# Kernel tuning notes

Measured on AMD Instinct MI355X. Metric: run time of the kernel, lower is better.

The kernel has to match this reference:

```python
import jax, jax.numpy as jnp
import numpy as np

ALPHA = 0.2  # LeakyReLU negative slope


def setup_inputs() -> dict:
    key = jax.random.key(0)
    k1, k2, k3, k4 = jax.random.split(key, 4)
    B, N, Fin, Fout = 8, 2048, 256, 256
    h = jax.random.normal(k1, (B, N, Fin), dtype=jnp.float32)
    # random 0/1 adjacency with guaranteed self-loops so every row has a neighbor
    adj = jax.random.randint(k2, (N, N), 0, 2).astype(jnp.float32)
    adj = jnp.maximum(adj, jnp.eye(N, dtype=jnp.float32))
    # xavier_uniform with gain=1.414
    def xavier(k, shape, gain=1.414):
        fan_in, fan_out = shape[0], shape[1]
        a = gain * np.sqrt(6.0 / (fan_in + fan_out))
        return jax.random.uniform(k, shape, dtype=jnp.float32, minval=-a, maxval=a)
    W = xavier(k3, (Fin, Fout))
    a = xavier(k4, (2 * Fout, 1))
    return {"h": h, "adj_matrix": adj, "W": W, "a": a}


def reference(h, adj_matrix, W, a):
    # h: [B, N, Fin], adj_matrix: [N, N], W: [Fin, Fout], a: [2*Fout, 1]
    Fout = W.shape[1]
    Wh = jnp.einsum("bnf,fo->bno", h, W)            # [B, N, Fout]
    a1, a2 = a[:Fout, 0], a[Fout:, 0]                 # split additive attention vector
    # e[b,i,j] = leakyrelu(Wh[b,i]@a1 + Wh[b,j]@a2) — equals concat([Wh_i,Wh_j])@a
    s1 = Wh @ a1                                      # [B, N]
    s2 = Wh @ a2                                      # [B, N]
    e = s1[:, :, None] + s2[:, None, :]               # [B, N, N]
    e = jnp.where(e >= 0, e, ALPHA * e)               # LeakyReLU
    e = jnp.where(adj_matrix[None] == 0, -jnp.inf, e)  # mask non-edges
    attention = jax.nn.softmax(e, axis=-1)            # [B, N, N]
    # dropout is identity in eval mode (training=False)
    h_prime = jnp.einsum("bij,bjo->bio", attention, Wh)
    return h_prime
```

## Files before the change

kernel.cpp:

```cpp
#include <hip/hip_runtime.h>
#include <cstdint>

#define NN 2048
#define LOG2E 1.4426950408889634f

typedef __attribute__((ext_vector_type(8))) short bf16x8;
typedef __attribute__((ext_vector_type(4))) float f32x4;

__device__ __forceinline__ unsigned short f2bf(float x){
  union { float f; unsigned u; } v; v.f = x;
  unsigned r = v.u + 0x7FFFu + ((v.u >> 16) & 1u);
  return (unsigned short)(r >> 16);
}
__device__ __forceinline__ unsigned pack2(float a, float b){
  return (unsigned)f2bf(a) | ((unsigned)f2bf(b) << 16);
}
__device__ __forceinline__ unsigned permpack(unsigned hi, unsigned lo){
  return __builtin_amdgcn_perm(hi, lo, 0x07060302u);
}

__global__ __launch_bounds__(256) void k_prep(const float* __restrict__ adj,
                                              const float* __restrict__ W,
                                              unsigned long long* __restrict__ ab,
                                              unsigned short* __restrict__ Wt){
  const int tid = threadIdx.x;
  const int bid = blockIdx.x;
  if (bid < 512){
    const int lane = tid & 63;
    unsigned* ab32 = (unsigned*)ab;
    #pragma unroll
    for (int r = 0; r < 4; r++){
      const int row = bid * 4 + r;
      #pragma unroll
      for (int part = 0; part < 2; part++){
        float4 v = ((const float4*)(adj + (size_t)row * NN))[part * 256 + tid];
        unsigned n = (v.x != 0.f ? 1u : 0u) | (v.y != 0.f ? 2u : 0u)
                   | (v.z != 0.f ? 4u : 0u) | (v.w != 0.f ? 8u : 0u);
        unsigned m;
        m = __shfl_xor(n, 1); n = (lane & 1) ? (m | (n << 4))  : (n | (m << 4));
        m = __shfl_xor(n, 2); n = (lane & 2) ? (m | (n << 8))  : (n | (m << 8));
        m = __shfl_xor(n, 4); n = (lane & 4) ? (m | (n << 16)) : (n | (m << 16));
        if ((lane & 7) == 0)
          ab32[row * 64 + part * 32 + (tid >> 3)] = n;
      }
    }
  } else {
    int g = (bid - 512) * 256 + tid;
    int o = g >> 8, k = g & 255;
    Wt[g] = f2bf(W[k * 256 + o]);
  }
}

__global__ __launch_bounds__(512, 2) void k_fused_gemm(const float* __restrict__ h,
                                                       const unsigned short* __restrict__ Wt,
                                                       const float* __restrict__ a,
                                                       unsigned short* __restrict__ WhT,
                                                       float* __restrict__ s1c,
                                                       float* __restrict__ s2c){
  __shared__ __align__(16) unsigned char As[2 * 8192];
  __shared__ __align__(16) unsigned short Ts[256 * 72];
  __shared__ float s1p[8][64], s2p[8][64];
  const int tid = threadIdx.x;
  const int r0 = blockIdx.x * 64;
  const int b  = r0 >> 11;
  const int i0 = r0 & (NN - 1);
  const int w = tid >> 6, lane = tid & 63, lhi = lane >> 4, llo = lane & 15;
  const int wc = w * 32;
  const int sit = w >> 1, skk = w & 1;
  const int srow = sit * 16 + llo;
  const int skol = skk * 32 + lhi * 8;

  f32x4 acc[4][2];
  #pragma unroll
  for (int i = 0; i < 4; i++)
    #pragma unroll
    for (int j = 0; j < 2; j++){ acc[i][j][0]=0.f; acc[i][j][1]=0.f; acc[i][j][2]=0.f; acc[i][j][3]=0.f; }

  float4 hv[4][2];
  #pragma unroll
  for (int t = 0; t < 4; t++){
    const float* hp = h + (size_t)(r0 + srow) * 256 + t * 64 + skol;
    hv[t][0] = *(const float4*)hp;
    hv[t][1] = *(const float4*)(hp + 4);
  }

  auto loadB = [&](int k0, bf16x8* dst){
    #pragma unroll
    for (int ot = 0; ot < 2; ot++)
      #pragma unroll
      for (int kk = 0; kk < 2; kk++)
        dst[ot * 2 + kk] = *(const bf16x8*)(Wt + (size_t)(wc + ot * 16 + llo) * 256 + k0 + kk * 32 + lhi * 8);
  };
  bf16x8 bfr[2][4];
  loadB(0, bfr[0]);

  #pragma unroll
  for (int t = 0; t < 4; t++){
    uint4 q = make_uint4(pack2(hv[t][0].x, hv[t][0].y), pack2(hv[t][0].z, hv[t][0].w),
                         pack2(hv[t][1].x, hv[t][1].y), pack2(hv[t][1].z, hv[t][1].w));
    *(uint4*)&As[(t & 1) * 8192 + w * 1024 + lane * 16] = q;
    __syncthreads();
    if (t < 3) loadB((t + 1) * 64, bfr[(t + 1) & 1]);
    bf16x8 af[2][4];
    #pragma unroll
    for (int kk = 0; kk < 2; kk++)
      #pragma unroll
      for (int it = 0; it < 4; it++)
        af[kk][it] = *(const bf16x8*)&As[(t & 1) * 8192 + (it * 2 + kk) * 1024 + lane * 16];
    #pragma unroll
    for (int kk = 0; kk < 2; kk++)
      #pragma unroll
      for (int it = 0; it < 4; it++)
        #pragma unroll
        for (int ot = 0; ot < 2; ot++)
          acc[it][ot] = __builtin_amdgcn_mfma_f32_16x16x32_bf16(af[kk][it], bfr[t & 1][ot * 2 + kk], acc[it][ot], 0, 0, 0);
  }

  float a1v[2], a2v[2];
  #pragma unroll
  for (int ot = 0; ot < 2; ot++){
    a1v[ot] = a[wc + ot * 16 + llo] * LOG2E;
    a2v[ot] = a[256 + wc + ot * 16 + llo] * LOG2E;
  }
  #pragma unroll
  for (int it = 0; it < 4; it++){
    #pragma unroll
    for (int q = 0; q < 4; q++){
      float p1 = acc[it][0][q] * a1v[0] + acc[it][1][q] * a1v[1];
      float p2 = acc[it][0][q] * a2v[0] + acc[it][1][q] * a2v[1];
      #pragma unroll
      for (int o = 1; o < 16; o <<= 1){ p1 += __shfl_xor(p1, o); p2 += __shfl_xor(p2, o); }
      if (llo == 0){
        s1p[w][it * 16 + lhi * 4 + q] = p1;
        s2p[w][it * 16 + lhi * 4 + q] = p2;
      }
    }
  }

  #pragma unroll
  for (int it = 0; it < 4; it++){
    #pragma unroll
    for (int ot = 0; ot < 2; ot++){
      int o = wc + ot * 16 + llo;
      uint2 u = make_uint2(pack2(acc[it][ot][0], acc[it][ot][1]),
                           pack2(acc[it][ot][2], acc[it][ot][3]));
      *(uint2*)&Ts[o * 72 + it * 16 + lhi * 4] = u;
    }
  }
  __syncthreads();

  if (tid < 64){
    float t1 = 0.f, t2 = 0.f;
    #pragma unroll
    for (int g = 0; g < 8; g++){ t1 += s1p[g][tid]; t2 += s2p[g][tid]; }
    s1c[r0 + tid] = t1;
    s2c[r0 + tid] = t2;
  }
  #pragma unroll
  for (int p = 0; p < 4; p++){
    int o = p * 64 + (tid >> 3), col = (tid & 7) * 8;
    *(uint4*)(WhT + (size_t)(b * 256 + o) * 2048 + i0 + col) = *(const uint4*)&Ts[o * 72 + col];
  }
}

__global__ __launch_bounds__(512, 2) void k_attn(const float* __restrict__ s1c,
                                                 const float* __restrict__ s2c,
                                                 const unsigned short* __restrict__ WhT,
                                                 const unsigned long long* __restrict__ ab,
                                                 float* __restrict__ out){
  __shared__ __align__(16) float E1s[2048];
  __shared__ __align__(16) float E2s[2048];
  __shared__ __align__(16) unsigned char Ps[65536];
  __shared__ __align__(16) unsigned char bitsB[64 * 264];
  __shared__ float s1s[64], lin[64], red[8], rsp[8][64];
  const int tid = threadIdx.x;
  const int bid = blockIdx.x;
  const int b = bid & 7, i0 = (bid >> 3) * 64;
  const int w = tid >> 6, lane = tid & 63, lhi = lane >> 4, llo = lane & 15;
  const int wc = w * 32;
  const int sit = w >> 1, skk = w & 1;
  const int sfrag = sit * 2 + skk;
  const int prow = sit * 16 + llo;

  auto loadB = [&](int j0, bf16x8* dst){
    #pragma unroll
    for (int ot = 0; ot < 2; ot++)
      #pragma unroll
      for (int kk = 0; kk < 2; kk++)
        dst[ot * 2 + kk] = *(const bf16x8*)(WhT + (size_t)(b * 256 + wc + ot * 16 + llo) * 2048 + j0 + kk * 32 + lhi * 8);
  };
  bf16x8 bA[4], bB[4];
  loadB(0, bA);

  float4 v = ((const float4*)(s2c + (size_t)b * NN))[tid];
  ((float4*)E1s)[tid] = make_float4(__builtin_amdgcn_exp2f(v.x), __builtin_amdgcn_exp2f(v.y),
                                    __builtin_amdgcn_exp2f(v.z), __builtin_amdgcn_exp2f(v.w));
  ((float4*)E2s)[tid] = make_float4(__builtin_amdgcn_exp2f(0.2f * v.x), __builtin_amdgcn_exp2f(0.2f * v.y),
                                    __builtin_amdgcn_exp2f(0.2f * v.z), __builtin_amdgcn_exp2f(0.2f * v.w));
  float vmax = fmaxf(fmaxf(v.x, v.y), fmaxf(v.z, v.w));
  #pragma unroll
  for (int o = 32; o; o >>= 1) vmax = fmaxf(vmax, __shfl_xor(vmax, o));
  if (lane == 0) red[w] = vmax;
  if (tid < 64) s1s[tid] = s1c[(size_t)b * NN + i0 + tid];
  #pragma unroll
  for (int k = 0; k < 4; k++){
    int g = k * 512 + tid;
    unsigned long long mw = ab[(size_t)i0 * 32 + g];
    *(unsigned long long*)&bitsB[(g >> 5) * 264 + (g & 31) * 8] = mw;
  }
  __syncthreads();
  float m2 = red[0];
  #pragma unroll
  for (int g = 1; g < 8; g++) m2 = fmaxf(m2, red[g]);

  const float s1v = s1s[prow];
  const float xm = s1v + m2;
  const float mv = fmaxf(xm, 0.2f * xm);
  const float k1 = __builtin_amdgcn_exp2f(s1v - mv);
  const float k2 = __builtin_amdgcn_exp2f(0.2f * s1v - mv);
  float rs = 0.f;

  f32x4 acc[4][2];
  #pragma unroll
  for (int i = 0; i < 4; i++)
    #pragma unroll
    for (int j = 0; j < 2; j++){ acc[i][j][0]=0.f; acc[i][j][1]=0.f; acc[i][j][2]=0.f; acc[i][j][3]=0.f; }

  unsigned puq[32];
  auto computeP = [&](int sN, int jc, unsigned* pq){
    const int j0 = sN * 512 + jc * 64 + skk * 32 + lhi * 8;
    unsigned bits = bitsB[prow * 264 + (j0 >> 3)];
    float4 xa = *(const float4*)&E1s[j0];
    float4 xb = *(const float4*)&E1s[j0 + 4];
    float4 ya = *(const float4*)&E2s[j0];
    float4 yb = *(const float4*)&E2s[j0 + 4];
    float e1[8] = {xa.x, xa.y, xa.z, xa.w, xb.x, xb.y, xb.z, xb.w};
    float e2[8] = {ya.x, ya.y, ya.z, ya.w, yb.x, yb.y, yb.z, yb.w};
    unsigned pu[8];
    #pragma unroll
    for (int e = 0; e < 8; e++){
      float p = fmaxf(e1[e] * k1, e2[e] * k2);
      unsigned m = ((bits >> e) & 1u) ? 0xFFFF0000u : 0u;
      unsigned u = __float_as_uint(p) & m;
      rs += __uint_as_float(u);
      pu[e] = u;
    }
    pq[0] = permpack(pu[1], pu[0]); pq[1] = permpack(pu[3], pu[2]);
    pq[2] = permpack(pu[5], pu[4]); pq[3] = permpack(pu[7], pu[6]);
  };

  #pragma unroll
  for (int jc = 0; jc < 8; jc++) computeP(0, jc, &puq[jc * 4]);

  for (int s = 0; s < 4; s++){
    if (s) __syncthreads();
    #pragma unroll
    for (int jc = 0; jc < 8; jc++)
      *(uint4*)&Ps[jc * 8192 + sfrag * 1024 + lane * 16] = *(const uint4*)&puq[jc * 4];
    __syncthreads();
    #pragma unroll
    for (int jc = 0; jc < 8; jc++){
      bf16x8 af[2][4];
      #pragma unroll
      for (int kk = 0; kk < 2; kk++)
        #pragma unroll
        for (int it = 0; it < 4; it++)
          af[kk][it] = *(const bf16x8*)&Ps[jc * 8192 + (it * 2 + kk) * 1024 + lane * 16];
      bf16x8* cur = (jc & 1) ? bB : bA;
      bf16x8* nxt = (jc & 1) ? bA : bB;
      if (jc < 7)       loadB((s * 8 + jc + 1) * 64, nxt);
      else if (s < 3)   loadB((s + 1) * 512, nxt);
      if (s < 3) computeP(s + 1, jc, &puq[jc * 4]);
      __builtin_amdgcn_s_setprio(1);
      #pragma unroll
      for (int kk = 0; kk < 2; kk++)
        #pragma unroll
        for (int it = 0; it < 4; it++)
          #pragma unroll
          for (int ot = 0; ot < 2; ot++)
            acc[it][ot] = __builtin_amdgcn_mfma_f32_16x16x32_bf16(af[kk][it], cur[ot * 2 + kk], acc[it][ot], 0, 0, 0);
      __builtin_amdgcn_s_setprio(0);
    }
  }

  rs += __shfl_xor(rs, 16);
  rs += __shfl_xor(rs, 32);
  if (lhi == 0) rsp[w][prow] = rs;
  __syncthreads();
  if (tid < 64){
    int it = tid >> 4;
    lin[tid] = 1.0f / (rsp[it * 2][tid] + rsp[it * 2 + 1][tid]);
  }
  __syncthreads();

  #pragma unroll
  for (int it = 0; it < 4; it++){
    #pragma unroll
    for (int ot = 0; ot < 2; ot++){
      int col = wc + ot * 16 + llo;
      #pragma unroll
      for (int q = 0; q < 4; q++){
        int row = it * 16 + lhi * 4 + q;
        out[(size_t)(b * NN + i0 + row) * 256 + col] = acc[it][ot][q] * lin[row];
      }
    }
  }
}

extern "C" void kernel_launch(void* const* d_in, const int* in_sizes, int n_in,
                              void* d_out, int out_size, void* d_ws, size_t ws_size,
                              hipStream_t stream) {
  const float* h   = (const float*)d_in[0];
  const float* adj = (const float*)d_in[1];
  const float* W   = (const float*)d_in[2];
  const float* a   = (const float*)d_in[3];
  float* out = (float*)d_out;

  char* ws = (char*)d_ws;
  unsigned short* WhT      = (unsigned short*)(ws);
  unsigned short* Wt       = (unsigned short*)(ws + 8388608);
  unsigned long long* ab   = (unsigned long long*)(ws + 8519680);
  float* s1c               = (float*)(ws + 9043968);
  float* s2c               = (float*)(ws + 9109504);

  hipLaunchKernelGGL(k_prep,       dim3(768), dim3(256), 0, stream, adj, W, ab, Wt);
  hipLaunchKernelGGL(k_fused_gemm, dim3(256), dim3(512), 0, stream, h, Wt, a, WhT, s1c, s2c);
  hipLaunchKernelGGL(k_attn,       dim3(256), dim3(512), 0, stream, s1c, s2c, WhT, ab, out);
}
```

Baseline: 130.9 us.

## Compute attention probabilities per wave in registers, drop LDS P exchange

Each wave now computes the bf16 attention-probability fragments for all 64 rows itself, straight from the E1/E2 tables and the adjacency bits, and feeds them directly into MFMA. This removes the 64KB shared-memory P buffer and its block-wide barriers. Row sums now come from an extra MFMA against a ones vector instead of a shuffle and LDS reduction. The trade is that the exp/mask/pack work is repeated in all 8 waves (8x more VALU work) plus 50% more MFMAs, in exchange for lower LDS use, which may allow higher occupancy, and no synchronisation.

```diff
diff --git a/kernel.cpp b/kernel.cpp
--- a/kernel.cpp
+++ b/kernel.cpp
@@ -170,17 +170,13 @@
                                                  float* __restrict__ out){
   __shared__ __align__(16) float E1s[2048];
   __shared__ __align__(16) float E2s[2048];
-  __shared__ __align__(16) unsigned char Ps[65536];
   __shared__ __align__(16) unsigned char bitsB[64 * 264];
-  __shared__ float s1s[64], lin[64], red[8], rsp[8][64];
+  __shared__ float s1s[64], red[8];
   const int tid = threadIdx.x;
   const int bid = blockIdx.x;
   const int b = bid & 7, i0 = (bid >> 3) * 64;
   const int w = tid >> 6, lane = tid & 63, lhi = lane >> 4, llo = lane & 15;
   const int wc = w * 32;
-  const int sit = w >> 1, skk = w & 1;
-  const int sfrag = sit * 2 + skk;
-  const int prow = sit * 16 + llo;
 
   auto loadB = [&](int j0, bf16x8* dst){
     #pragma unroll
@@ -213,95 +209,80 @@
   #pragma unroll
   for (int g = 1; g < 8; g++) m2 = fmaxf(m2, red[g]);
 
-  const float s1v = s1s[prow];
-  const float xm = s1v + m2;
-  const float mv = fmaxf(xm, 0.2f * xm);
-  const float k1 = __builtin_amdgcn_exp2f(s1v - mv);
-  const float k2 = __builtin_amdgcn_exp2f(0.2f * s1v - mv);
-  float rs = 0.f;
-
-  f32x4 acc[4][2];
-  #pragma unroll
-  for (int i = 0; i < 4; i++)
+  float k1v[4], k2v[4];
+  #pragma unroll
+  for (int it = 0; it < 4; it++){
+    float s1v = s1s[it * 16 + llo];
+    float xm = s1v + m2;
+    float mv = fmaxf(xm, 0.2f * xm);
+    k1v[it] = __builtin_amdgcn_exp2f(s1v - mv);
+    k2v[it] = __builtin_amdgcn_exp2f(0.2f * s1v - mv);
+  }
+
+  f32x4 acc[4][2], accr[4];
+  #pragma unroll
+  for (int i = 0; i < 4; i++){
+    accr[i][0]=0.f; accr[i][1]=0.f; accr[i][2]=0.f; accr[i][3]=0.f;
     #pragma unroll
     for (int j = 0; j < 2; j++){ acc[i][j][0]=0.f; acc[i][j][1]=0.f; acc[i][j][2]=0.f; acc[i][j][3]=0.f; }
-
-  unsigned puq[32];
-  auto computeP = [&](int sN, int jc, unsigned* pq){
-    const int j0 = sN * 512 + jc * 64 + skk * 32 + lhi * 8;
-    unsigned bits = bitsB[prow * 264 + (j0 >> 3)];
-    float4 xa = *(const float4*)&E1s[j0];
-    float4 xb = *(const float4*)&E1s[j0 + 4];
-    float4 ya = *(const float4*)&E2s[j0];
-    float4 yb = *(const float4*)&E2s[j0 + 4];
-    float e1[8] = {xa.x, xa.y, xa.z, xa.w, xb.x, xb.y, xb.z, xb.w};
-    float e2[8] = {ya.x, ya.y, ya.z, ya.w, yb.x, yb.y, yb.z, yb.w};
-    unsigned pu[8];
-    #pragma unroll
-    for (int e = 0; e < 8; e++){
-      float p = fmaxf(e1[e] * k1, e2[e] * k2);
-      unsigned m = ((bits >> e) & 1u) ? 0xFFFF0000u : 0u;
-      unsigned u = __float_as_uint(p) & m;
-      rs += __uint_as_float(u);
-      pu[e] = u;
-    }
-    pq[0] = permpack(pu[1], pu[0]); pq[1] = permpack(pu[3], pu[2]);
-    pq[2] = permpack(pu[5], pu[4]); pq[3] = permpack(pu[7], pu[6]);
+  }
+  bf16x8 onesB;
+  { union { unsigned u[4]; bf16x8 v2; } t;
+    t.u[0]=0x3F803F80u; t.u[1]=0x3F803F80u; t.u[2]=0x3F803F80u; t.u[3]=0x3F803F80u;
+    onesB = t.v2; }
+
+  auto chunkBody = [&](int jc, bf16x8* curB, bf16x8* nxtB, bool pf){
+    unsigned long long bw[4];
+    #pragma unroll
+    for (int it = 0; it < 4; it++)
+      bw[it] = *(const unsigned long long*)&bitsB[(it * 16 + llo) * 264 + jc * 8];
+    if (pf) loadB((jc + 1) * 64, nxtB);
+    #pragma unroll
+    for (int kk = 0; kk < 2; kk++){
+      const int j0 = jc * 64 + kk * 32 + lhi * 8;
+      float4 xa = *(const float4*)&E1s[j0];
+      float4 xb = *(const float4*)&E1s[j0 + 4];
+      float4 ya = *(const float4*)&E2s[j0];
+      float4 yb = *(const float4*)&E2s[j0 + 4];
+      float e1[8] = {xa.x, xa.y, xa.z, xa.w, xb.x, xb.y, xb.z, xb.w};
+      float e2[8] = {ya.x, ya.y, ya.z, ya.w, yb.x, yb.y, yb.z, yb.w};
+      #pragma unroll
+      for (int it = 0; it < 4; it++){
+        unsigned b8 = (unsigned)(bw[it] >> ((kk * 4 + lhi) * 8)) & 0xFFu;
+        unsigned pu[8];
+        #pragma unroll
+        for (int e = 0; e < 8; e++){
+          float p = fmaxf(e1[e] * k1v[it], e2[e] * k2v[it]);
+          unsigned m = ((b8 >> e) & 1u) ? 0xFFFF0000u : 0u;
+          pu[e] = __float_as_uint(p) & m;
+        }
+        union { unsigned u[4]; bf16x8 v2; } afu;
+        afu.u[0] = permpack(pu[1], pu[0]); afu.u[1] = permpack(pu[3], pu[2]);
+        afu.u[2] = permpack(pu[5], pu[4]); afu.u[3] = permpack(pu[7], pu[6]);
+        acc[it][0] = __builtin_amdgcn_mfma_f32_16x16x32_bf16(afu.v2, curB[kk],     acc[it][0], 0, 0, 0);
+        acc[it][1] = __builtin_amdgcn_mfma_f32_16x16x32_bf16(afu.v2, curB[2 + kk], acc[it][1], 0, 0, 0);
+        accr[it]   = __builtin_amdgcn_mfma_f32_16x16x32_bf16(afu.v2, onesB,        accr[it],   0, 0, 0);
+      }
+    }
   };
 
-  #pragma unroll
-  for (int jc = 0; jc < 8; jc++) computeP(0, jc, &puq[jc * 4]);
-
-  for (int s = 0; s < 4; s++){
-    if (s) __syncthreads();
-    #pragma unroll
-    for (int jc = 0; jc < 8; jc++)
-      *(uint4*)&Ps[jc * 8192 + sfrag * 1024 + lane * 16] = *(const uint4*)&puq[jc * 4];
-    __syncthreads();
-    #pragma unroll
-    for (int jc = 0; jc < 8; jc++){
-      bf16x8 af[2][4];
-      #pragma unroll
-      for (int kk = 0; kk < 2; kk++)
-        #pragma unroll
-        for (int it = 0; it < 4; it++)
-          af[kk][it] = *(const bf16x8*)&Ps[jc * 8192 + (it * 2 + kk) * 1024 + lane * 16];
-      bf16x8* cur = (jc & 1) ? bB : bA;
-      bf16x8* nxt = (jc & 1) ? bA : bB;
-      if (jc < 7)       loadB((s * 8 + jc + 1) * 64, nxt);
-      else if (s < 3)   loadB((s + 1) * 512, nxt);
-      if (s < 3) computeP(s + 1, jc, &puq[jc * 4]);
-      __builtin_amdgcn_s_setprio(1);
-      #pragma unroll
-      for (int kk = 0; kk < 2; kk++)
-        #pragma unroll
-        for (int it = 0; it < 4; it++)
-          #pragma unroll
-          for (int ot = 0; ot < 2; ot++)
-            acc[it][ot] = __builtin_amdgcn_mfma_f32_16x16x32_bf16(af[kk][it], cur[ot * 2 + kk], acc[it][ot], 0, 0, 0);
-      __builtin_amdgcn_s_setprio(0);
-    }
-  }
-
-  rs += __shfl_xor(rs, 16);
-  rs += __shfl_xor(rs, 32);
-  if (lhi == 0) rsp[w][prow] = rs;
-  __syncthreads();
-  if (tid < 64){
-    int it = tid >> 4;
-    lin[tid] = 1.0f / (rsp[it * 2][tid] + rsp[it * 2 + 1][tid]);
-  }
-  __syncthreads();
+  for (int jc2 = 0; jc2 < 32; jc2 += 2){
+    chunkBody(jc2,     bA, bB, true);
+    chunkBody(jc2 + 1, bB, bA, jc2 + 1 < 31);
+  }
 
   #pragma unroll
   for (int it = 0; it < 4; it++){
+    f32x4 linv;
+    #pragma unroll
+    for (int q = 0; q < 4; q++) linv[q] = 1.0f / accr[it][q];
     #pragma unroll
     for (int ot = 0; ot < 2; ot++){
       int col = wc + ot * 16 + llo;
       #pragma unroll
       for (int q = 0; q < 4; q++){
         int row = it * 16 + lhi * 4 + q;
-        out[(size_t)(b * NN + i0 + row) * 256 + col] = acc[it][ot][q] * lin[row];
+        out[(size_t)(b * NN + i0 + row) * 256 + col] = acc[it][ot][q] * linv[q];
       }
     }
   }
```

Result: slower. 142.6 us (+8.9%).
